# Kernel tuning notes

Measured on AMD Instinct MI355X. Metric: run time of the kernel, lower is better.

## Reference

```python
import jax, jax.numpy as jnp
import numpy as np

B, N, C, D, K = 8, 4096, 64, 64, 16


def _knn_indices(features, k):
    # so topk-smallest indices match torch.cdist + topk(largest=False))
    sq = jnp.sum(features * features, axis=-1)                      # [B, N]
    d2 = sq[:, :, None] + sq[:, None, :] - 2.0 * jnp.einsum('bic,bjc->bij', features, features)
    n = features.shape[1]
    eye = jnp.eye(n, dtype=bool)[None]                              # mask self
    d2 = jnp.where(eye, jnp.inf, d2)
    _, idx = jax.lax.top_k(-d2, k)                                  # k smallest
    return idx                                                      # [B, N, k]


def setup_inputs() -> dict:
    key = jax.random.key(0)
    k0, k1, k2 = jax.random.split(key, 3)
    features = jax.random.normal(k0, (B, N, C), dtype=jnp.float32)
    W1 = jax.random.normal(k1, (2 * C, D), dtype=jnp.float32) * 0.05
    b1 = jnp.zeros((D,), dtype=jnp.float32)
    W2 = jax.random.normal(k2, (D, D), dtype=jnp.float32) * 0.05
    b2 = jnp.zeros((D,), dtype=jnp.float32)
    return {"features": features, "W1": W1, "b1": b1, "W2": W2, "b2": b2}


def reference(features, W1, b1, W2, b2):
    idx = _knn_indices(features, K)                                 # [B, N, K]
    neighbors = jax.vmap(lambda f, i: f[i])(features, idx)          # [B, N, K, C]
    central = features[:, :, None, :]                               # [B, N, 1, C]
    edge = jnp.concatenate(
        [jnp.broadcast_to(central, neighbors.shape), neighbors - central], axis=-1
    )                                                               # [B, N, K, 2C]
    h = jax.nn.gelu(edge @ W1 + b1, approximate=False)              # exact GELU (torch default)
    h = jax.nn.gelu(h @ W2 + b2, approximate=False)                 # [B, N, K, D]
    return jnp.max(h, axis=2)                                       # [B, N, D]
```

## Files before the change

kernel.cpp:

```cpp
#include <hip/hip_runtime.h>
#include <math.h>
#include <stdint.h>

#define B 8
#define N 4096
#define C 64
#define D 64
#define K 16

typedef __attribute__((ext_vector_type(8))) short short8;
typedef __attribute__((ext_vector_type(4))) float f32x4;

__device__ __forceinline__ unsigned short f2bf(float x) {
    unsigned u = __float_as_uint(x);
    unsigned r = (u + 0x7FFFu + ((u >> 16) & 1u)) >> 16;
    return (unsigned short)r;
}
__device__ __forceinline__ float bf2f(unsigned short h) {
    return __uint_as_float(((unsigned)h) << 16);
}

__device__ __forceinline__ double pack_key(float d2, unsigned idx) {
    uint2 u; u.x = idx; u.y = __float_as_uint(d2);
    return __builtin_bit_cast(double, u);
}

__global__ __launch_bounds__(256)
void prep_kernel(const float* __restrict__ F, float* __restrict__ sq,
                 unsigned short* __restrict__ HP, unsigned short* __restrict__ MP,
                 unsigned short* __restrict__ LP) {
    const int row = blockIdx.x * 256 + threadIdx.x;
    const float4* src = (const float4*)(F + (size_t)row * C);
    float4 v[16];
    #pragma unroll
    for (int q = 0; q < 16; q++) v[q] = src[q];

    {
        float r[8];
        #pragma unroll
        for (int j = 0; j < 8; j++) {
            float t = ((const float*)v)[j];
            r[j] = t * t;
        }
        #pragma unroll
        for (int m = 1; m < 8; m++) {
            #pragma unroll
            for (int j = 0; j < 8; j++) {
                float t = ((const float*)v)[8 * m + j];
                r[j] = fmaf(t, t, r[j]);
            }
        }
        sq[row] = ((r[0] + r[1]) + (r[2] + r[3])) + ((r[4] + r[5]) + (r[6] + r[7]));
    }

    uint4* dh = (uint4*)(HP + (size_t)row * C);
    uint4* dm = (uint4*)(MP + (size_t)row * C);
    uint4* dl = (uint4*)(LP + (size_t)row * C);
    #pragma unroll
    for (int c8 = 0; c8 < 8; c8++) {
        unsigned hq[4], mq[4], lq[4];
        #pragma unroll
        for (int e = 0; e < 4; e++) {
            float x0 = ((const float*)v)[c8 * 8 + 2 * e];
            float x1 = ((const float*)v)[c8 * 8 + 2 * e + 1];
            unsigned short h0 = f2bf(x0), h1 = f2bf(x1);
            float r10 = x0 - bf2f(h0), r11 = x1 - bf2f(h1);
            unsigned short m0 = f2bf(r10), m1 = f2bf(r11);
            float r20 = r10 - bf2f(m0), r21 = r11 - bf2f(m1);
            unsigned short l0 = f2bf(r20), l1 = f2bf(r21);
            hq[e] = (unsigned)h0 | ((unsigned)h1 << 16);
            mq[e] = (unsigned)m0 | ((unsigned)m1 << 16);
            lq[e] = (unsigned)l0 | ((unsigned)l1 << 16);
        }
        dh[c8] = make_uint4(hq[0], hq[1], hq[2], hq[3]);
        dm[c8] = make_uint4(mq[0], mq[1], mq[2], mq[3]);
        dl[c8] = make_uint4(lq[0], lq[1], lq[2], lq[3]);
    }
}

__device__ __forceinline__ void merge4_store(const uint64_t* __restrict__ keys,
                                             int qloc, uint64_t* __restrict__ dst) {
    const uint64_t* K0 = keys + (qloc * 4 + 0) * 16;
    const uint64_t* K1 = keys + (qloc * 4 + 1) * 16;
    const uint64_t* K2 = keys + (qloc * 4 + 2) * 16;
    const uint64_t* K3 = keys + (qloc * 4 + 3) * 16;
    int p0 = 0, p1 = 0, p2 = 0, p3 = 0;
    uint64_t h0 = K0[0], h1 = K1[0], h2 = K2[0], h3 = K3[0];
    #pragma unroll
    for (int k = 0; k < K; k++) {
        uint64_t m01 = h0 < h1 ? h0 : h1;
        uint64_t m23 = h2 < h3 ? h2 : h3;
        uint64_t mv  = m01 < m23 ? m01 : m23;
        dst[k] = mv;
        if      (mv == h0) { ++p0; h0 = (p0 < 16) ? K0[p0] : ~0ull; }
        else if (mv == h1) { ++p1; h1 = (p1 < 16) ? K1[p1] : ~0ull; }
        else if (mv == h2) { ++p2; h2 = (p2 < 16) ? K2[p2] : ~0ull; }
        else               { ++p3; h3 = (p3 < 16) ? K3[p3] : ~0ull; }
    }
}

__global__ __launch_bounds__(512, 2)
void knn_mfma_kernel(const unsigned short* __restrict__ HP,
                     const unsigned short* __restrict__ MP,
                     const unsigned short* __restrict__ LP,
                     const float* __restrict__ sqg, uint64_t* __restrict__ keysg) {
    __shared__ __align__(16) char lds[49152];

    const int s  = blockIdx.y;
    const int b  = blockIdx.z;
    const int i0 = blockIdx.x * 128;
    const int c0 = s * 2048;
    const unsigned short* Hb = HP + (size_t)b * N * C;
    const unsigned short* Mb = MP + (size_t)b * N * C;
    const unsigned short* Lb = LP + (size_t)b * N * C;
    const float* sqb = sqg + (size_t)b * N;

    const int tid = threadIdx.x;
    const int l   = tid & 63;
    const int w   = tid >> 6;

    const int lr  = tid >> 3;
    const int lq  = tid & 7;
    const int wbyte = (lr * 128 + lq * 16) ^ ((lr & 7) << 4);

    const double KMAX = __builtin_bit_cast(double, 0x7FEFFFFFFFFFFFFFull);

    uint4 ph, pm, pl;
    {
        const size_t rb = (size_t)(c0 + lr) * C + lq * 8;
        ph = *(const uint4*)(Hb + rb);
        pm = *(const uint4*)(Mb + rb);
        pl = *(const uint4*)(Lb + rb);
    }

    {
        const size_t r0 = (size_t)(i0 + lr) * C + lq * 8;
        const size_t r1 = (size_t)(i0 + 64 + lr) * C + lq * 8;
        uint4 qh0 = *(const uint4*)(Hb + r0), qh1 = *(const uint4*)(Hb + r1);
        uint4 qm0 = *(const uint4*)(Mb + r0), qm1 = *(const uint4*)(Mb + r1);
        uint4 ql0 = *(const uint4*)(Lb + r0), ql1 = *(const uint4*)(Lb + r1);
        *(uint4*)(lds +              wbyte) = qh0;
        *(uint4*)(lds +  8192      + wbyte) = qm0;
        *(uint4*)(lds + 16384      + wbyte) = ql0;
        *(uint4*)(lds + 24576      + wbyte) = qh1;
        *(uint4*)(lds + 24576+8192 + wbyte) = qm1;
        *(uint4*)(lds + 24576+16384+ wbyte) = ql1;
    }
    __syncthreads();

    const int koff = (l >> 4) * 16;
    const int swzR = (l & 7) << 4;
    const int qrow = w * 16 + (l & 15);
    const char* qbuf = lds + ((qrow >> 6) ? 24576 : 0);
    const int qr6 = qrow & 63;
    const int qb0 = (qr6 * 128 + koff) ^ swzR;
    const int qb1 = (qr6 * 128 + 64 + koff) ^ swzR;
    short8 bh0 = *(const short8*)(qbuf + qb0),         bh1 = *(const short8*)(qbuf + qb1);
    short8 bm0 = *(const short8*)(qbuf +  8192 + qb0), bm1 = *(const short8*)(qbuf +  8192 + qb1);
    short8 bl0 = *(const short8*)(qbuf + 16384 + qb0), bl1 = *(const short8*)(qbuf + 16384 + qb1);

    const float sqq   = sqb[i0 + qrow];
    const int   qglob = i0 + qrow;
    const int   crow0 = (l >> 4) * 4;
    const int   dtile = i0 + ((w >> 2) << 6);

    __syncthreads();

    *(uint4*)(lds +         wbyte) = ph;
    *(uint4*)(lds +  8192 + wbyte) = pm;
    *(uint4*)(lds + 16384 + wbyte) = pl;
    {
        const size_t rb = (size_t)(c0 + 64 + lr) * C + lq * 8;
        ph = *(const uint4*)(Hb + rb);
        pm = *(const uint4*)(Mb + rb);
        pl = *(const uint4*)(Lb + rb);
    }
    __syncthreads();

    double bd[16];
    #pragma unroll
    for (int k = 0; k < 16; k++) bd[k] = KMAX;

    for (int t = 0; t < 32; t++) {
        const int j0 = c0 + t * 64;
        char* bufA = lds + ((t & 1) ? 24576 : 0);
        char* bufB = lds + ((t & 1) ? 0 : 24576);

        if (t < 31) {
            *(uint4*)(bufB +         wbyte) = ph;
            *(uint4*)(bufB +  8192 + wbyte) = pm;
            *(uint4*)(bufB + 16384 + wbyte) = pl;
        }
        if (t < 30) {
            const size_t rb = (size_t)(j0 + 128 + lr) * C + lq * 8;
            ph = *(const uint4*)(Hb + rb);
            pm = *(const uint4*)(Mb + rb);
            pl = *(const uint4*)(Lb + rb);
        }

        float4 sqm0 = *(const float4*)(sqb + j0 +      crow0);
        float4 sqm1 = *(const float4*)(sqb + j0 + 16 + crow0);
        float4 sqm2 = *(const float4*)(sqb + j0 + 32 + crow0);
        float4 sqm3 = *(const float4*)(sqb + j0 + 48 + crow0);

        double nk[16];

        #pragma unroll
        for (int m = 0; m < 4; m++) {
            const int arow = m * 16 + (l & 15);
            const int ab0 = (arow * 128 + koff) ^ swzR;
            const int ab1 = (arow * 128 + 64 + koff) ^ swzR;
            short8 ah0 = *(const short8*)(bufA + ab0);
            short8 ah1 = *(const short8*)(bufA + ab1);
            short8 am0 = *(const short8*)(bufA + 8192 + ab0);
            short8 am1 = *(const short8*)(bufA + 8192 + ab1);
            short8 al0 = *(const short8*)(bufA + 16384 + ab0);
            short8 al1 = *(const short8*)(bufA + 16384 + ab1);

            f32x4 acc1 = {0.f, 0.f, 0.f, 0.f};
            acc1 = __builtin_amdgcn_mfma_f32_16x16x32_bf16(am0, bm0, acc1, 0, 0, 0);
            acc1 = __builtin_amdgcn_mfma_f32_16x16x32_bf16(am1, bm1, acc1, 0, 0, 0);
            acc1 = __builtin_amdgcn_mfma_f32_16x16x32_bf16(ah0, bl0, acc1, 0, 0, 0);
            acc1 = __builtin_amdgcn_mfma_f32_16x16x32_bf16(ah1, bl1, acc1, 0, 0, 0);
            acc1 = __builtin_amdgcn_mfma_f32_16x16x32_bf16(al0, bh0, acc1, 0, 0, 0);
            f32x4 acc2 = {0.f, 0.f, 0.f, 0.f};
            acc2 = __builtin_amdgcn_mfma_f32_16x16x32_bf16(al1, bh1, acc2, 0, 0, 0);
            acc2 = __builtin_amdgcn_mfma_f32_16x16x32_bf16(ah0, bm0, acc2, 0, 0, 0);
            acc2 = __builtin_amdgcn_mfma_f32_16x16x32_bf16(ah1, bm1, acc2, 0, 0, 0);
            acc2 = __builtin_amdgcn_mfma_f32_16x16x32_bf16(am0, bh0, acc2, 0, 0, 0);
            acc2 = __builtin_amdgcn_mfma_f32_16x16x32_bf16(am1, bh1, acc2, 0, 0, 0);
            f32x4 acch = {0.f, 0.f, 0.f, 0.f};
            acch = __builtin_amdgcn_mfma_f32_16x16x32_bf16(ah0, bh0, acch, 0, 0, 0);
            acch = __builtin_amdgcn_mfma_f32_16x16x32_bf16(ah1, bh1, acch, 0, 0, 0);

            float4 sqm = (m == 0) ? sqm0 : (m == 1) ? sqm1 : (m == 2) ? sqm2 : sqm3;
            #pragma unroll
            for (int r = 0; r < 4; r++) {
                float sqc = (r == 0) ? sqm.x : (r == 1) ? sqm.y : (r == 2) ? sqm.z : sqm.w;
                float gg = acch[r] + (acc1[r] + acc2[r]);
                float d2 = fmaf(-2.0f, gg, sqq + sqc);
                d2 = fmaxf(d2, 0.0f);
                nk[m * 4 + r] = pack_key(d2, (unsigned)(j0 + m * 16 + crow0 + r));
            }
        }

        if (j0 == dtile) {
            #pragma unroll
            for (int m = 0; m < 4; m++)
                #pragma unroll
                for (int r = 0; r < 4; r++)
                    if ((j0 + m * 16 + crow0 + r) == qglob) nk[m * 4 + r] = KMAX;
        }

        #pragma unroll
        for (int p = 1; p < 16; p <<= 1) {
            #pragma unroll
            for (int kk = p; kk >= 1; kk >>= 1) {
                #pragma unroll
                for (int j = kk % p; j <= 16 - 1 - kk; j += 2 * kk) {
                    #pragma unroll
                    for (int i = 0; i <= ((kk - 1 < 16 - j - kk - 1) ? kk - 1 : 16 - j - kk - 1); i++) {
                        if ((i + j) / (2 * p) == (i + j + kk) / (2 * p)) {
                            double a = nk[i + j], c2 = nk[i + j + kk];
                            nk[i + j]      = fmax(a, c2);
                            nk[i + j + kk] = fmin(a, c2);
                        }
                    }
                }
            }
        }
        #pragma unroll
        for (int i = 0; i < 16; i++) bd[i] = fmin(bd[i], nk[i]);
        #pragma unroll
        for (int j = 8; j > 0; j >>= 1) {
            #pragma unroll
            for (int i = 0; i < 16; i++) {
                int ixj = i ^ j;
                if (ixj > i) {
                    double a = bd[i], c2 = bd[ixj];
                    bd[i]   = fmin(a, c2);
                    bd[ixj] = fmax(a, c2);
                }
            }
        }

        __syncthreads();
    }

    uint64_t* keys = (uint64_t*)lds;
    if (w < 4) {
        const int qloc = w * 16 + (l & 15);
        const int base = (qloc * 4 + (l >> 4)) * 16;
        #pragma unroll
        for (int k = 0; k < 16; k++)
            keys[base + k] = __builtin_bit_cast(uint64_t, bd[k]);
    }
    __syncthreads();
    if (tid < 64)
        merge4_store(keys, tid, keysg + ((size_t)b * N + i0 + tid) * 32 + s * 16);
    __syncthreads();
    if (w >= 4) {
        const int qloc = (w - 4) * 16 + (l & 15);
        const int base = (qloc * 4 + (l >> 4)) * 16;
        #pragma unroll
        for (int k = 0; k < 16; k++)
            keys[base + k] = __builtin_bit_cast(uint64_t, bd[k]);
    }
    __syncthreads();
    if (tid < 64)
        merge4_store(keys, tid, keysg + ((size_t)b * N + i0 + 64 + tid) * 32 + s * 16);
}

__global__ __launch_bounds__(256)
void knn_merge_kernel(const uint64_t* __restrict__ keysg, int* __restrict__ knn) {
    const int q = blockIdx.x * 256 + threadIdx.x;
    const uint64_t* A  = keysg + (size_t)q * 32;
    const uint64_t* Bp = A + 16;
    int pa = 0, pb = 0;
    uint64_t ha = A[0], hb = Bp[0];
    int* dst = knn + (size_t)q * K;
    #pragma unroll
    for (int k = 0; k < K; k++) {
        uint64_t mv = ha < hb ? ha : hb;
        dst[k] = (int)(mv & 0xFFFFFFFFu);
        if (mv == ha) { ++pa; ha = (pa < 16) ? A[pa] : ~0ull; }
        else          { ++pb; hb = (pb < 16) ? Bp[pb] : ~0ull; }
    }
}

__device__ __forceinline__ float gelu_fast(float x) {
    float az = fabsf(x) * 0.70710678118654752440f;
    float t  = __builtin_amdgcn_rcpf(fmaf(0.3275911f, az, 1.0f));
    float p  = t * fmaf(t, fmaf(t, fmaf(t, fmaf(t, 1.061405429f, -1.453152027f),
                                        1.421413741f), -0.284496736f), 0.254829592f);
    float e  = p * __builtin_amdgcn_exp2f(-az * az * 1.44269504088896f);
    float g  = 0.5f * x;
    return (x >= 0.0f) ? g * (2.0f - e) : g * e;
}

#define QPW 4

__global__ __launch_bounds__(256)
void mlp_mfma_kernel(const float* __restrict__ F,
                     const unsigned short* __restrict__ HP,
                     const unsigned short* __restrict__ MP,
                     const int* __restrict__ knn,
                     const float* __restrict__ W1, const float* __restrict__ b1,
                     const float* __restrict__ W2, const float* __restrict__ b2,
                     float* __restrict__ out) {
    __shared__ __align__(16) unsigned short W1h[64 * 128];
    __shared__ __align__(16) unsigned short W1m[64 * 128];
    __shared__ __align__(16) unsigned short hbh[4][1024];

    const int tid = threadIdx.x;
    const int l   = tid & 63;
    const int w   = tid >> 6;

    const int cb    = (l >> 4) * 8;
    const int swzL  = (l & 15) << 4;
    const int qbase = (blockIdx.x * 4 + w) * QPW;
    char* hbh_w = (char*)&hbh[w][0];

    int nbs[QPW];
    #pragma unroll
    for (int jq = 0; jq < QPW; jq++)
        nbs[jq] = knn[(size_t)(qbase + jq) * K + (l & 15)];

    for (int e = tid; e < 8192; e += 256) {
        const int n = e & 63, k = e >> 6;
        const int srcrow = (k < 64) ? (64 + k) : (k - 64);
        float x = W1[srcrow * 64 + n];
        unsigned short hh = f2bf(x);
        unsigned short mm = f2bf(x - bf2f(hh));
        const int byte = (n * 256 + k * 2) ^ ((n & 15) << 4);
        *(unsigned short*)((char*)W1h + byte) = hh;
        *(unsigned short*)((char*)W1m + byte) = mm;
    }

    short8 B2h[4][2];
    float b1v[4], b2v[4];
    {
        const int n = (l & 15);
        #pragma unroll
        for (int nt = 0; nt < 4; nt++) {
            const int nn = nt * 16 + n;
            b1v[nt] = b1[nn];
            b2v[nt] = b2[nn];
            #pragma unroll
            for (int c = 0; c < 2; c++) {
                const int k0 = c * 32 + (l >> 4) * 8;
                short8 vh;
                #pragma unroll
                for (int jj = 0; jj < 8; jj++)
                    vh[jj] = (short)f2bf(W2[(k0 + jj) * 64 + nn]);
                B2h[nt][c] = vh;
            }
        }
    }
    __syncthreads();

    float4 pnA0[2], pnA1[2], pnB0[2], pnB1[2];
#define LOADN(s_, jq_) { \
        const int q_ = qbase + (jq_); \
        const float* Fb_ = F + (size_t)(q_ >> 12) * N * C; \
        const size_t nr_ = (size_t)nbs[jq_] * C; \
        pnA0[s_] = *(const float4*)(Fb_ + nr_ + cb); \
        pnA1[s_] = *(const float4*)(Fb_ + nr_ + cb + 4); \
        pnB0[s_] = *(const float4*)(Fb_ + nr_ + 32 + cb); \
        pnB1[s_] = *(const float4*)(Fb_ + nr_ + 36 + cb); \
    }
    LOADN(0, 0);

    #pragma unroll
    for (int jq = 0; jq < QPW; jq++) {
        const int sbuf = jq & 1;
        if (jq + 1 < QPW) LOADN(sbuf ^ 1, jq + 1);

        const int q  = qbase + jq;
        const int b  = q >> 12;
        const int ci = q & (N - 1);
        const float*          Fb  = F  + (size_t)b * N * C;
        const unsigned short* HPb = HP + (size_t)b * N * C;
        const unsigned short* MPb = MP + (size_t)b * N * C;

        float4 cA0 = *(const float4*)(Fb + (size_t)ci * C + cb);
        float4 cA1 = *(const float4*)(Fb + (size_t)ci * C + cb + 4);
        float4 cB0 = *(const float4*)(Fb + (size_t)ci * C + 32 + cb);
        float4 cB1 = *(const float4*)(Fb + (size_t)ci * C + 36 + cb);
        float4 nA0 = pnA0[sbuf], nA1 = pnA1[sbuf];
        float4 nB0 = pnB0[sbuf], nB1 = pnB1[sbuf];

        short8 ach0 = *(const short8*)(HPb + (size_t)ci * C + cb);
        short8 ach1 = *(const short8*)(HPb + (size_t)ci * C + 32 + cb);
        short8 acm0 = *(const short8*)(MPb + (size_t)ci * C + cb);
        short8 acm1 = *(const short8*)(MPb + (size_t)ci * C + 32 + cb);

        short8 adh0, adm0, adh1, adm1;
        {
            float d0[8] = {nA0.x - cA0.x, nA0.y - cA0.y, nA0.z - cA0.z, nA0.w - cA0.w,
                           nA1.x - cA1.x, nA1.y - cA1.y, nA1.z - cA1.z, nA1.w - cA1.w};
            float d1[8] = {nB0.x - cB0.x, nB0.y - cB0.y, nB0.z - cB0.z, nB0.w - cB0.w,
                           nB1.x - cB1.x, nB1.y - cB1.y, nB1.z - cB1.z, nB1.w - cB1.w};
            #pragma unroll
            for (int jj = 0; jj < 8; jj++) {
                unsigned short h0 = f2bf(d0[jj]);
                adh0[jj] = (short)h0; adm0[jj] = (short)f2bf(d0[jj] - bf2f(h0));
                unsigned short h1 = f2bf(d1[jj]);
                adh1[jj] = (short)h1; adm1[jj] = (short)f2bf(d1[jj] - bf2f(h1));
            }
        }

        #pragma unroll
        for (int nt = 0; nt < 4; nt++) {
            const int rowb = (nt * 16 + (l & 15)) * 256 + (l >> 4) * 16;
            f32x4 a1 = {0.f, 0.f, 0.f, 0.f};
            f32x4 a2 = {0.f, 0.f, 0.f, 0.f};
            #pragma unroll
            for (int kc = 0; kc < 4; kc++) {
                const int byte = (rowb + kc * 64) ^ swzL;
                short8 Bh = *(const short8*)((char*)W1h + byte);
                short8 Bm = *(const short8*)((char*)W1m + byte);
                short8 Ah = (kc == 0) ? adh0 : (kc == 1) ? adh1 : (kc == 2) ? ach0 : ach1;
                short8 Am = (kc == 0) ? adm0 : (kc == 1) ? adm1 : (kc == 2) ? acm0 : acm1;
                a1 = __builtin_amdgcn_mfma_f32_16x16x32_bf16(Ah, Bh, a1, 0, 0, 0);
                a2 = __builtin_amdgcn_mfma_f32_16x16x32_bf16(Ah, Bm, a2, 0, 0, 0);
                a2 = __builtin_amdgcn_mfma_f32_16x16x32_bf16(Am, Bh, a2, 0, 0, 0);
            }
            #pragma unroll
            for (int r = 0; r < 4; r++) {
                const int row = (l >> 4) * 4 + r;
                const int col = nt * 16 + (l & 15);
                float hv = gelu_fast(a1[r] + a2[r] + b1v[nt]);
                const int byte = (row * 128 + col * 2) ^ ((row & 7) << 4);
                *(unsigned short*)(hbh_w + byte) = f2bf(hv);
            }
        }

        asm volatile("s_waitcnt lgkmcnt(0)" ::: "memory");
        __builtin_amdgcn_sched_barrier(0);

        short8 Ah2[2];
        #pragma unroll
        for (int kc = 0; kc < 2; kc++) {
            const int byte = ((l & 15) * 128 + kc * 64 + (l >> 4) * 16) ^ (((l & 15) & 7) << 4);
            Ah2[kc] = *(const short8*)(hbh_w + byte);
        }
        #pragma unroll
        for (int nt = 0; nt < 4; nt++) {
            f32x4 a1 = {0.f, 0.f, 0.f, 0.f};
            #pragma unroll
            for (int kc = 0; kc < 2; kc++)
                a1 = __builtin_amdgcn_mfma_f32_16x16x32_bf16(Ah2[kc], B2h[nt][kc], a1, 0, 0, 0);
            float mx = -INFINITY;
            #pragma unroll
            for (int r = 0; r < 4; r++)
                mx = fmaxf(mx, gelu_fast(a1[r] + b2v[nt]));
            mx = fmaxf(mx, __shfl_xor(mx, 16));
            mx = fmaxf(mx, __shfl_xor(mx, 32));
            if (l < 16) out[(size_t)q * D + nt * 16 + l] = mx;
        }
    }
#undef LOADN
}

extern "C" void kernel_launch(void* const* d_in, const int* in_sizes, int n_in,
                              void* d_out, int out_size, void* d_ws, size_t ws_size,
                              hipStream_t stream) {
    const float* F  = (const float*)d_in[0];
    const float* W1 = (const float*)d_in[1];
    const float* b1 = (const float*)d_in[2];
    const float* W2 = (const float*)d_in[3];
    const float* b2 = (const float*)d_in[4];
    float* out = (float*)d_out;

    char* ws = (char*)d_ws;
    float*          sq   = (float*)ws;
    uint64_t*       keys = (uint64_t*)(ws + (128 << 10));
    unsigned short* HP   = (unsigned short*)(ws + (8320 << 10));
    unsigned short* MP   = (unsigned short*)(ws + (12416 << 10));
    unsigned short* LP   = (unsigned short*)(ws + (16512 << 10));
    int*            knn  = (int*)LP;

    prep_kernel<<<dim3(B * N / 256), 256, 0, stream>>>(F, sq, HP, MP, LP);
    knn_mfma_kernel<<<dim3(N / 128, 2, B), 512, 0, stream>>>(HP, MP, LP, sq, keys);
    knn_merge_kernel<<<dim3(B * N / 256), 256, 0, stream>>>(keys, knn);
    mlp_mfma_kernel<<<dim3(B * N / (4 * QPW)), 256, 0, stream>>>(
        F, HP, MP, knn, W1, b1, W2, b2, out);
}
```

Before: 256.0 us.

## Split KNN candidate range four ways and prefetch central rows in MLP

The KNN distance kernel now splits each query's candidate range into four chunks of 1024 instead of two of 2048, doubling the grid to improve occupancy and load balance. Partial top-16 lists go to two buffers, one of which reuses the output buffer as scratch, and the merge kernel becomes a 4-way merge. The MLP kernel also double-buffers the central point's fp32 and bf16 loads together with the neighbor loads to hide latency. The cost is more partial-key traffic, a costlier merge, more registers in the MLP loop, and reliance on the output buffer being large enough and overwritten later.

```diff
diff --git a/kernel.cpp b/kernel.cpp
--- a/kernel.cpp
+++ b/kernel.cpp
@@ -103,13 +103,14 @@
 void knn_mfma_kernel(const unsigned short* __restrict__ HP,
                      const unsigned short* __restrict__ MP,
                      const unsigned short* __restrict__ LP,
-                     const float* __restrict__ sqg, uint64_t* __restrict__ keysg) {
+                     const float* __restrict__ sqg,
+                     uint64_t* __restrict__ keysgA, uint64_t* __restrict__ keysgB) {
     __shared__ __align__(16) char lds[49152];
 
     const int s  = blockIdx.y;
     const int b  = blockIdx.z;
     const int i0 = blockIdx.x * 128;
-    const int c0 = s * 2048;
+    const int c0 = s * 1024;
     const unsigned short* Hb = HP + (size_t)b * N * C;
     const unsigned short* Mb = MP + (size_t)b * N * C;
     const unsigned short* Lb = LP + (size_t)b * N * C;
@@ -181,17 +182,17 @@
     #pragma unroll
     for (int k = 0; k < 16; k++) bd[k] = KMAX;
 
-    for (int t = 0; t < 32; t++) {
+    for (int t = 0; t < 16; t++) {
         const int j0 = c0 + t * 64;
         char* bufA = lds + ((t & 1) ? 24576 : 0);
         char* bufB = lds + ((t & 1) ? 0 : 24576);
 
-        if (t < 31) {
+        if (t < 15) {
             *(uint4*)(bufB +         wbyte) = ph;
             *(uint4*)(bufB +  8192 + wbyte) = pm;
             *(uint4*)(bufB + 16384 + wbyte) = pl;
         }
-        if (t < 30) {
+        if (t < 14) {
             const size_t rb = (size_t)(j0 + 128 + lr) * C + lq * 8;
             ph = *(const uint4*)(Hb + rb);
             pm = *(const uint4*)(Mb + rb);
@@ -288,6 +289,8 @@
     }
 
     uint64_t* keys = (uint64_t*)lds;
+    uint64_t* base0 = (s < 2) ? keysgA : keysgB;
+    const int  soff = (s & 1) * 16;
     if (w < 4) {
         const int qloc = w * 16 + (l & 15);
         const int base = (qloc * 4 + (l >> 4)) * 16;
@@ -297,7 +300,7 @@
     }
     __syncthreads();
     if (tid < 64)
-        merge4_store(keys, tid, keysg + ((size_t)b * N + i0 + tid) * 32 + s * 16);
+        merge4_store(keys, tid, base0 + ((size_t)b * N + i0 + tid) * 32 + soff);
     __syncthreads();
     if (w >= 4) {
         const int qloc = (w - 4) * 16 + (l & 15);
@@ -308,23 +311,30 @@
     }
     __syncthreads();
     if (tid < 64)
-        merge4_store(keys, tid, keysg + ((size_t)b * N + i0 + 64 + tid) * 32 + s * 16);
+        merge4_store(keys, tid, base0 + ((size_t)b * N + i0 + 64 + tid) * 32 + soff);
 }
 
 __global__ __launch_bounds__(256)
-void knn_merge_kernel(const uint64_t* __restrict__ keysg, int* __restrict__ knn) {
+void knn_merge_kernel(const uint64_t* __restrict__ keysgA,
+                      const uint64_t* __restrict__ keysgB, int* __restrict__ knn) {
     const int q = blockIdx.x * 256 + threadIdx.x;
-    const uint64_t* A  = keysg + (size_t)q * 32;
-    const uint64_t* Bp = A + 16;
-    int pa = 0, pb = 0;
-    uint64_t ha = A[0], hb = Bp[0];
+    const uint64_t* P0 = keysgA + (size_t)q * 32;
+    const uint64_t* P1 = P0 + 16;
+    const uint64_t* P2 = keysgB + (size_t)q * 32;
+    const uint64_t* P3 = P2 + 16;
+    int p0 = 0, p1 = 0, p2 = 0, p3 = 0;
+    uint64_t h0 = P0[0], h1 = P1[0], h2 = P2[0], h3 = P3[0];
     int* dst = knn + (size_t)q * K;
     #pragma unroll
     for (int k = 0; k < K; k++) {
-        uint64_t mv = ha < hb ? ha : hb;
+        uint64_t m01 = h0 < h1 ? h0 : h1;
+        uint64_t m23 = h2 < h3 ? h2 : h3;
+        uint64_t mv  = m01 < m23 ? m01 : m23;
         dst[k] = (int)(mv & 0xFFFFFFFFu);
-        if (mv == ha) { ++pa; ha = (pa < 16) ? A[pa] : ~0ull; }
-        else          { ++pb; hb = (pb < 16) ? Bp[pb] : ~0ull; }
+        if      (mv == h0) { ++p0; h0 = (p0 < 16) ? P0[p0] : ~0ull; }
+        else if (mv == h1) { ++p1; h1 = (p1 < 16) ? P1[p1] : ~0ull; }
+        else if (mv == h2) { ++p2; h2 = (p2 < 16) ? P2[p2] : ~0ull; }
+        else               { ++p3; h3 = (p3 < 16) ? P3[p3] : ~0ull; }
     }
 }
 
@@ -400,40 +410,44 @@
     __syncthreads();
 
     float4 pnA0[2], pnA1[2], pnB0[2], pnB1[2];
-#define LOADN(s_, jq_) { \
-        const int q_ = qbase + (jq_); \
-        const float* Fb_ = F + (size_t)(q_ >> 12) * N * C; \
+    float4 pcA0[2], pcA1[2], pcB0[2], pcB1[2];
+    short8 pah0[2], pah1[2], pam0[2], pam1[2];
+#define LOADQ(s_, jq_) { \
+        const int q_  = qbase + (jq_); \
+        const int b_  = q_ >> 12; \
+        const int ci_ = q_ & (N - 1); \
+        const float*          Fb_  = F  + (size_t)b_ * N * C; \
+        const unsigned short* HPb_ = HP + (size_t)b_ * N * C; \
+        const unsigned short* MPb_ = MP + (size_t)b_ * N * C; \
         const size_t nr_ = (size_t)nbs[jq_] * C; \
         pnA0[s_] = *(const float4*)(Fb_ + nr_ + cb); \
         pnA1[s_] = *(const float4*)(Fb_ + nr_ + cb + 4); \
         pnB0[s_] = *(const float4*)(Fb_ + nr_ + 32 + cb); \
         pnB1[s_] = *(const float4*)(Fb_ + nr_ + 36 + cb); \
-    }
-    LOADN(0, 0);
+        pcA0[s_] = *(const float4*)(Fb_ + (size_t)ci_ * C + cb); \
+        pcA1[s_] = *(const float4*)(Fb_ + (size_t)ci_ * C + cb + 4); \
+        pcB0[s_] = *(const float4*)(Fb_ + (size_t)ci_ * C + 32 + cb); \
+        pcB1[s_] = *(const float4*)(Fb_ + (size_t)ci_ * C + 36 + cb); \
+        pah0[s_] = *(const short8*)(HPb_ + (size_t)ci_ * C + cb); \
+        pah1[s_] = *(const short8*)(HPb_ + (size_t)ci_ * C + 32 + cb); \
+        pam0[s_] = *(const short8*)(MPb_ + (size_t)ci_ * C + cb); \
+        pam1[s_] = *(const short8*)(MPb_ + (size_t)ci_ * C + 32 + cb); \
+    }
+    LOADQ(0, 0);
 
     #pragma unroll
     for (int jq = 0; jq < QPW; jq++) {
         const int sbuf = jq & 1;
-        if (jq + 1 < QPW) LOADN(sbuf ^ 1, jq + 1);
-
-        const int q  = qbase + jq;
-        const int b  = q >> 12;
-        const int ci = q & (N - 1);
-        const float*          Fb  = F  + (size_t)b * N * C;
-        const unsigned short* HPb = HP + (size_t)b * N * C;
-        const unsigned short* MPb = MP + (size_t)b * N * C;
-
-        float4 cA0 = *(const float4*)(Fb + (size_t)ci * C + cb);
-        float4 cA1 = *(const float4*)(Fb + (size_t)ci * C + cb + 4);
-        float4 cB0 = *(const float4*)(Fb + (size_t)ci * C + 32 + cb);
-        float4 cB1 = *(const float4*)(Fb + (size_t)ci * C + 36 + cb);
+        if (jq + 1 < QPW) LOADQ(sbuf ^ 1, jq + 1);
+
+        const int q = qbase + jq;
+
+        float4 cA0 = pcA0[sbuf], cA1 = pcA1[sbuf];
+        float4 cB0 = pcB0[sbuf], cB1 = pcB1[sbuf];
         float4 nA0 = pnA0[sbuf], nA1 = pnA1[sbuf];
         float4 nB0 = pnB0[sbuf], nB1 = pnB1[sbuf];
-
-        short8 ach0 = *(const short8*)(HPb + (size_t)ci * C + cb);
-        short8 ach1 = *(const short8*)(HPb + (size_t)ci * C + 32 + cb);
-        short8 acm0 = *(const short8*)(MPb + (size_t)ci * C + cb);
-        short8 acm1 = *(const short8*)(MPb + (size_t)ci * C + 32 + cb);
+        short8 ach0 = pah0[sbuf], ach1 = pah1[sbuf];
+        short8 acm0 = pam0[sbuf], acm1 = pam1[sbuf];
 
         short8 adh0, adm0, adh1, adm1;
         {
@@ -500,7 +514,7 @@
             if (l < 16) out[(size_t)q * D + nt * 16 + l] = mx;
         }
     }
-#undef LOADN
+#undef LOADQ
 }
 
 extern "C" void kernel_launch(void* const* d_in, const int* in_sizes, int n_in,
@@ -514,16 +528,17 @@
     float* out = (float*)d_out;
 
     char* ws = (char*)d_ws;
-    float*          sq   = (float*)ws;
-    uint64_t*       keys = (uint64_t*)(ws + (128 << 10));
-    unsigned short* HP   = (unsigned short*)(ws + (8320 << 10));
-    unsigned short* MP   = (unsigned short*)(ws + (12416 << 10));
-    unsigned short* LP   = (unsigned short*)(ws + (16512 << 10));
-    int*            knn  = (int*)LP;
+    float*          sq    = (float*)ws;
+    uint64_t*       keysA = (uint64_t*)(ws + (128 << 10));
+    uint64_t*       keysB = (uint64_t*)d_out;
+    unsigned short* HP    = (unsigned short*)(ws + (8320 << 10));
+    unsigned short* MP    = (unsigned short*)(ws + (12416 << 10));
+    unsigned short* LP    = (unsigned short*)(ws + (16512 << 10));
+    int*            knn   = (int*)LP;
 
     prep_kernel<<<dim3(B * N / 256), 256, 0, stream>>>(F, sq, HP, MP, LP);
-    knn_mfma_kernel<<<dim3(N / 128, 2, B), 512, 0, stream>>>(HP, MP, LP, sq, keys);
-    knn_merge_kernel<<<dim3(B * N / 256), 256, 0, stream>>>(keys, knn);
+    knn_mfma_kernel<<<dim3(N / 128, 4, B), 512, 0, stream>>>(HP, MP, LP, sq, keysA, keysB);
+    knn_merge_kernel<<<dim3(B * N / 256), 256, 0, stream>>>(keysA, keysB, knn);
     mlp_mfma_kernel<<<dim3(B * N / (4 * QPW)), 256, 0, stream>>>(
         F, HP, MP, knn, W1, b1, W2, b2, out);
 }
```

After: 266.8 us. 4.2% more time.
